# Kernel tuning notes

Measured on AMD Instinct MI355X. Metric: run time of the kernel, lower is better.

The kernel has to match this reference:

```python
import jax, jax.numpy as jnp
import numpy as np

B, CIN, COUT, H, W_ = 8, 48, 64, 224, 224
KS, PAD = 3, 1
BN_EPS = 1e-5
TWO_PI = 2.0 * np.pi


def _ste(hard, soft):
    # forward value = hard, gradient flows through soft
    return soft + jax.lax.stop_gradient(hard - soft)


def channel_adaptive_bypass(x, out_ch):
    in_ch = x.shape[1]
    repeat, merge = out_ch // in_ch, out_ch % in_ch
    b, _, h, w = x.shape
    parts = []
    if repeat > 0:
        parts.append(jnp.tile(x, (1, repeat, 1, 1)))
    if merge > 0:
        regular = in_ch // merge * (merge - 1)
        parts.append(x[:, :regular].reshape(b, -1, merge - 1, h, w).mean(axis=1))
        parts.append(x[:, regular:].reshape(b, -1, 1, h, w).mean(axis=1))
    return jnp.concatenate(parts, axis=1)


def setup_inputs() -> dict:
    key = jax.random.key(0)
    ks = jax.random.split(key, 2)
    x = jax.random.normal(ks[0], (B, CIN, H, W_), dtype=jnp.float32)
    weight = 0.001 * jax.random.normal(ks[1], (COUT, CIN, KS, KS), dtype=jnp.float32)
    return {
        'x': x,
        'alpha': jnp.ones((1,), jnp.float32),
        'epsilon': jnp.zeros((1, CIN, 1, 1), jnp.float32),
        'tau': jnp.ones((1, CIN, 1, 1), jnp.float32),
        'A': jnp.ones((1, CIN, 1, 1), jnp.float32),
        'weight': weight,
        'gamma': jnp.ones((COUT,), jnp.float32),
        'beta': jnp.zeros((COUT,), jnp.float32),
    }


def reference(x, alpha, epsilon, tau, A, weight, gamma, beta):
    inp = x
    # PeriodicBinarizer: sin-based periodic binarization with tanh STE
    z = (x - epsilon) / tau * TWO_PI
    s = jnp.sin(z)
    xa = _ste(jnp.sign(s), jnp.tanh(s * alpha)) * A
    # BinaryWeightConv2d: per-filter mean-|w| scaled sign weights, clip STE
    scale = jax.lax.stop_gradient(jnp.mean(jnp.abs(weight), axis=(1, 2, 3), keepdims=True))
    bw = _ste(scale * jnp.sign(weight), jnp.clip(weight, -1.0, 1.0))
    y = jax.lax.conv_general_dilated(
        xa, bw, window_strides=(1, 1), padding=((PAD, PAD), (PAD, PAD)),
        dimension_numbers=('NCHW', 'OIHW', 'NCHW'))
    # BatchNorm2d (training mode: batch statistics, biased variance)
    mu = jnp.mean(y, axis=(0, 2, 3), keepdims=True)
    var = jnp.var(y, axis=(0, 2, 3), keepdims=True)
    yn = (y - mu) * jax.lax.rsqrt(var + BN_EPS)
    yn = yn * gamma[None, :, None, None] + beta[None, :, None, None]
    return yn + channel_adaptive_bypass(inp, COUT)
```

## Files before the change

### kernel.cpp

```cpp
#include <hip/hip_runtime.h>
#include <math.h>

#define BB   8
#define CI   48
#define CO   64
#define HH   224
#define WW   224
#define HW   50176
#define NPC  (BB*HW)
#define HP   226
#define WP   226
#define PADW (HP*WP)

typedef unsigned long long u64;
typedef unsigned int u32;

constexpr float TWO_PI_F = 6.283185307179586476925286766559f;

constexpr size_t YOFF  = 0;
constexpr size_t XBOFF = YOFF  + (size_t)BB*CO*HW*2;
constexpr size_t WBOFF = XBOFF + (size_t)BB*PADW*8;
constexpr size_t S2OFF = WBOFF + (size_t)CO*9*8;
constexpr size_t CROFF = S2OFF + CO*8;
constexpr size_t SAOFF = CROFF + 9*CO*4;
constexpr size_t S1OFF = SAOFF + CO*4;

static_assert(S2OFF % 8 == 0, "S2 must be 8B-aligned for u64 atomicAdd");

__global__ __launch_bounds__(64) void k_prep(const float* __restrict__ w,
                                             const float* __restrict__ A,
                                             u64* __restrict__ wb, float* __restrict__ sA,
                                             int* __restrict__ corr,
                                             int* __restrict__ S1, u64* __restrict__ S2) {
    const int o = blockIdx.x;
    const int i = threadIdx.x;
    float wv[9];
    double acc = 0.0;
    if (i < CI) {
        #pragma unroll
        for (int k = 0; k < 9; ++k) {
            wv[k] = w[(size_t)(o * CI + i) * 9 + k];
            acc += fabs((double)wv[k]);
        }
    } else {
        #pragma unroll
        for (int k = 0; k < 9; ++k) wv[k] = 0.0f;
    }
    #pragma unroll
    for (int m = 32; m > 0; m >>= 1) acc += __shfl_xor(acc, m, 64);
    u64 bits[9];
    int wpop[9];
    #pragma unroll
    for (int k = 0; k < 9; ++k) {
        bits[k] = __ballot(i < CI && wv[k] > 0.0f);
        wpop[k] = __popcll(bits[k]);
    }
    if (i == 0) {
        sA[o] = (float)(acc / 432.0) * A[0];
        S1[o] = 0;
        S2[o] = 0ull;
        #pragma unroll
        for (int k = 0; k < 9; ++k) wb[o * 9 + k] = bits[k];
    }
    if (i < 9) {
        const int rc = i / 3, cc = i - rc * 3;
        int nv = 0, ws = 0;
        #pragma unroll
        for (int k = 0; k < 9; ++k) {
            const int r = k / 3, kc = k - r * 3;
            const bool inv = (rc == 0 && r == 0) || (rc == 2 && r == 2) ||
                             (cc == 0 && kc == 0) || (cc == 2 && kc == 2);
            if (inv) ws += wpop[k]; else ++nv;
        }
        corr[i * CO + o] = 48 * nv + 2 * ws;
    }
}

__global__ __launch_bounds__(256) void k_pack(const float* __restrict__ x,
                                              const float* __restrict__ eps,
                                              const float* __restrict__ tau,
                                              u64* __restrict__ xbp) {
    const int t = blockIdx.x * 256 + threadIdx.x;
    if (t < BB * 900) {
        const int b = t / 900, j = t - b * 900;
        int r, c;
        if (j < 226)      { r = 0;             c = j; }
        else if (j < 452) { r = 225;           c = j - 226; }
        else if (j < 676) { r = 1 + (j - 452); c = 0; }
        else              { r = 1 + (j - 676); c = 225; }
        xbp[(size_t)b * PADW + r * WP + c] = 0ull;
    }
    const int b = t / HW;
    const int p = t - b * HW;
    const int h = p / WW, w = p - h * WW;
    const float* xp = x + (size_t)b * CI * HW + p;
    u64 w0 = 0;
    for (int c = 0; c < CI; ++c) {
        const float v = xp[(size_t)c * HW];
        if (sinf((v - eps[c]) / tau[c] * TWO_PI_F) > 0.0f) w0 |= (1ull << c);
    }
    xbp[(size_t)b * PADW + (size_t)(h + 1) * WP + (w + 1)] = w0;
}

__global__ __launch_bounds__(256) void k_conv(const u64* __restrict__ xbp,
                                              const u64* __restrict__ wbg,
                                              const int* __restrict__ corrg,
                                              short* __restrict__ y) {
    __shared__ u64 wbs[CO * 9];
    __shared__ int cs[9 * CO];
    const int tid = threadIdx.x;
    for (int i = tid; i < CO * 9; i += 256) wbs[i] = wbg[i];
    for (int i = tid; i < 9 * CO; i += 256) cs[i] = corrg[i];
    __syncthreads();

    const int t = blockIdx.x * 256 + tid;
    const int b = t / (HW / 2);
    const int pr = t - b * (HW / 2);
    const int p = pr * 2;
    const int h = p / WW, w = p - h * WW;

    const u64* xp = xbp + (size_t)b * PADW + (size_t)h * WP + w;
    u64 win[3][4];
    #pragma unroll
    for (int r = 0; r < 3; ++r)
        #pragma unroll
        for (int c = 0; c < 4; ++c)
            win[r][c] = xp[r * WP + c];

    const int rc  = (h == 0) ? 0 : ((h == HH - 1) ? 2 : 1);
    const int ci0 = (rc * 3 + ((w == 0) ? 0 : 1)) * CO;
    const int ci1 = (rc * 3 + ((w + 1 == WW - 1) ? 2 : 1)) * CO;

    short* yp = y + (size_t)b * CO * HW + p;
    #pragma unroll 2
    for (int o = 0; o < CO; ++o) {
        const u64* wo = &wbs[o * 9];
        int d0 = 0, d1 = 0;
        #pragma unroll
        for (int r = 0; r < 3; ++r) {
            #pragma unroll
            for (int k = 0; k < 3; ++k) {
                const u64 wk = wo[r * 3 + k];
                d0 += __popcll(win[r][k] ^ wk);
                d1 += __popcll(win[r][k + 1] ^ wk);
            }
        }
        const int cnt0 = cs[ci0 + o] - 2 * d0;
        const int cnt1 = cs[ci1 + o] - 2 * d1;
        *(short2*)(yp + (size_t)o * HW) = make_short2((short)cnt0, (short)cnt1);
    }
}

__global__ __launch_bounds__(256) void k_stats(const short* __restrict__ y,
                                               int* __restrict__ S1,
                                               u64* __restrict__ S2) {
    const int o = blockIdx.x >> 3;
    const int part = blockIdx.x & 7;
    const int tid = threadIdx.x;
    int s1 = 0;
    u32 s2 = 0;
    for (int b = 0; b < BB; ++b) {
        const int4* yp = (const int4*)(y + ((size_t)b * CO + o) * HW);
        for (int v = part * 784 + tid; v < (part + 1) * 784; v += 256) {
            const int4 q = yp[v];
            int u;
            u = q.x; { const int a = (u << 16) >> 16, c = u >> 16; s1 += a + c; s2 += (u32)(a*a + c*c); }
            u = q.y; { const int a = (u << 16) >> 16, c = u >> 16; s1 += a + c; s2 += (u32)(a*a + c*c); }
            u = q.z; { const int a = (u << 16) >> 16, c = u >> 16; s1 += a + c; s2 += (u32)(a*a + c*c); }
            u = q.w; { const int a = (u << 16) >> 16, c = u >> 16; s1 += a + c; s2 += (u32)(a*a + c*c); }
        }
    }
    __shared__ long long r1[256];
    __shared__ long long r2[256];
    r1[tid] = s1;
    r2[tid] = (long long)s2;
    __syncthreads();
    for (int st = 128; st > 0; st >>= 1) {
        if (tid < st) { r1[tid] += r1[tid + st]; r2[tid] += r2[tid + st]; }
        __syncthreads();
    }
    if (tid == 0) {
        atomicAdd(&S1[o], (int)r1[0]);
        atomicAdd((unsigned long long*)&S2[o], (u64)r2[0]);
    }
}

__global__ __launch_bounds__(256) void k_final(const float* __restrict__ x,
                                               const short* __restrict__ y,
                                               const int* __restrict__ S1,
                                               const u64* __restrict__ S2,
                                               const float* __restrict__ sA,
                                               const float* __restrict__ gam,
                                               const float* __restrict__ bta,
                                               float* __restrict__ out) {
    __shared__ float sh[2];
    const int o = blockIdx.y, b = blockIdx.z;
    if (threadIdx.x == 0) {
        const double m1 = (double)S1[o] / (double)NPC;
        const double m2 = (double)(long long)S2[o] / (double)NPC;
        const double vr = m2 - m1 * m1;
        const float s = sA[o];
        const float var = (float)((double)s * (double)s * vr);
        const float inv = (float)(1.0 / sqrt((double)var + (double)1e-5f));
        sh[0] = s * inv * gam[o];
        sh[1] = bta[o] - (float)(s * m1) * inv * gam[o];
    }
    __syncthreads();
    const float ca = sh[0], cb = sh[1];

    const int p = blockIdx.x * 1024 + threadIdx.x * 4;
    const short4 yv = *(const short4*)(y + ((size_t)b * CO + o) * HW + p);
    float4 r;
    r.x = fmaf(ca, (float)yv.x, cb);
    r.y = fmaf(ca, (float)yv.y, cb);
    r.z = fmaf(ca, (float)yv.z, cb);
    r.w = fmaf(ca, (float)yv.w, cb);

    const float* xb_ = x + (size_t)b * CI * HW + p;
    if (o < CI) {
        const float4 xv = *(const float4*)(xb_ + (size_t)o * HW);
        r.x += xv.x; r.y += xv.y; r.z += xv.z; r.w += xv.w;
    } else {
        const int j = o - CI;
        const int c0 = (j < 15) ? j      : 45;
        const int c1 = (j < 15) ? j + 15 : 46;
        const int c2 = (j < 15) ? j + 30 : 47;
        const float4 x0 = *(const float4*)(xb_ + (size_t)c0 * HW);
        const float4 x1 = *(const float4*)(xb_ + (size_t)c1 * HW);
        const float4 x2 = *(const float4*)(xb_ + (size_t)c2 * HW);
        r.x += (x0.x + x1.x + x2.x) * (1.0f / 3.0f);
        r.y += (x0.y + x1.y + x2.y) * (1.0f / 3.0f);
        r.z += (x0.z + x1.z + x2.z) * (1.0f / 3.0f);
        r.w += (x0.w + x1.w + x2.w) * (1.0f / 3.0f);
    }
    *(float4*)(out + ((size_t)b * CO + o) * HW + p) = r;
}

extern "C" void kernel_launch(void* const* d_in, const int* in_sizes, int n_in,
                              void* d_out, int out_size, void* d_ws, size_t ws_size,
                              hipStream_t stream) {
    const float* x     = (const float*)d_in[0];
    const float* eps   = (const float*)d_in[2];
    const float* tau   = (const float*)d_in[3];
    const float* A     = (const float*)d_in[4];
    const float* w     = (const float*)d_in[5];
    const float* gamma = (const float*)d_in[6];
    const float* beta  = (const float*)d_in[7];
    float* out = (float*)d_out;

    char* ws = (char*)d_ws;
    short* y    = (short*)(ws + YOFF);
    u64*   xbp  = (u64*)(ws + XBOFF);
    u64*   wb   = (u64*)(ws + WBOFF);
    u64*   S2   = (u64*)(ws + S2OFF);
    int*   corr = (int*)(ws + CROFF);
    float* sA   = (float*)(ws + SAOFF);
    int*   S1   = (int*)(ws + S1OFF);

    k_prep <<<CO, 64, 0, stream>>>(w, A, wb, sA, corr, S1, S2);
    k_pack <<<NPC / 256, 256, 0, stream>>>(x, eps, tau, xbp);
    k_conv <<<NPC / 2 / 256, 256, 0, stream>>>(xbp, wb, corr, y);
    k_stats<<<CO * 8, 256, 0, stream>>>(y, S1, S2);
    k_final<<<dim3(HW / 1024, CO, BB), 256, 0, stream>>>(x, y, S1, S2, sA, gamma, beta, out);
}
```

Baseline: 278.5 us.

## Fuse BN statistics into binary conv and pack two pixels per thread

Removes the separate statistics kernel by accumulating per-channel sum and sum of squares inside the conv kernel, using shared-memory atomics spread over 32 slots and then one global atomic per channel per block. This avoids re-reading the int16 conv output from memory. The pack kernel also now handles two adjacent pixels per thread with float2 loads, halving its grid. The cost is two shared atomics per output channel per thread in the conv inner loop, plus extra shared memory that may reduce occupancy.

```diff
diff --git a/kernel.cpp b/kernel.cpp
--- a/kernel.cpp
+++ b/kernel.cpp
@@ -90,27 +90,41 @@
         else              { r = 1 + (j - 676); c = 225; }
         xbp[(size_t)b * PADW + r * WP + c] = 0ull;
     }
-    const int b = t / HW;
-    const int p = t - b * HW;
+    const int b = t / (HW / 2);
+    const int pr = t - b * (HW / 2);
+    const int p = pr * 2;
     const int h = p / WW, w = p - h * WW;
-    const float* xp = x + (size_t)b * CI * HW + p;
-    u64 w0 = 0;
+    u64 w0 = 0, w1 = 0;
     for (int c = 0; c < CI; ++c) {
-        const float v = xp[(size_t)c * HW];
-        if (sinf((v - eps[c]) / tau[c] * TWO_PI_F) > 0.0f) w0 |= (1ull << c);
-    }
-    xbp[(size_t)b * PADW + (size_t)(h + 1) * WP + (w + 1)] = w0;
+        const float2 v = *(const float2*)(x + ((size_t)b * CI + c) * HW + p);
+        const float e = eps[c], tu = tau[c];
+        const u64 bit = 1ull << c;
+        if (sinf((v.x - e) / tu * TWO_PI_F) > 0.0f) w0 |= bit;
+        if (sinf((v.y - e) / tu * TWO_PI_F) > 0.0f) w1 |= bit;
+    }
+    u64* d = xbp + (size_t)b * PADW + (size_t)(h + 1) * WP + (w + 1);
+    d[0] = w0;
+    d[1] = w1;
 }
 
 __global__ __launch_bounds__(256) void k_conv(const u64* __restrict__ xbp,
                                               const u64* __restrict__ wbg,
                                               const int* __restrict__ corrg,
-                                              short* __restrict__ y) {
+                                              short* __restrict__ y,
+                                              int* __restrict__ S1,
+                                              u64* __restrict__ S2) {
     __shared__ u64 wbs[CO * 9];
     __shared__ int cs[9 * CO];
+    __shared__ int ls1[CO][32];
+    __shared__ u32 ls2[CO][32];
     const int tid = threadIdx.x;
     for (int i = tid; i < CO * 9; i += 256) wbs[i] = wbg[i];
     for (int i = tid; i < 9 * CO; i += 256) cs[i] = corrg[i];
+    {
+        int* z1 = &ls1[0][0];
+        u32* z2 = &ls2[0][0];
+        for (int i = tid; i < CO * 32; i += 256) { z1[i] = 0; z2[i] = 0u; }
+    }
     __syncthreads();
 
     const int t = blockIdx.x * 256 + tid;
@@ -131,6 +145,7 @@
     const int ci0 = (rc * 3 + ((w == 0) ? 0 : 1)) * CO;
     const int ci1 = (rc * 3 + ((w + 1 == WW - 1) ? 2 : 1)) * CO;
 
+    const int slot = tid & 31;
     short* yp = y + (size_t)b * CO * HW + p;
     #pragma unroll 2
     for (int o = 0; o < CO; ++o) {
@@ -148,40 +163,17 @@
         const int cnt0 = cs[ci0 + o] - 2 * d0;
         const int cnt1 = cs[ci1 + o] - 2 * d1;
         *(short2*)(yp + (size_t)o * HW) = make_short2((short)cnt0, (short)cnt1);
-    }
-}
-
-__global__ __launch_bounds__(256) void k_stats(const short* __restrict__ y,
-                                               int* __restrict__ S1,
-                                               u64* __restrict__ S2) {
-    const int o = blockIdx.x >> 3;
-    const int part = blockIdx.x & 7;
-    const int tid = threadIdx.x;
-    int s1 = 0;
-    u32 s2 = 0;
-    for (int b = 0; b < BB; ++b) {
-        const int4* yp = (const int4*)(y + ((size_t)b * CO + o) * HW);
-        for (int v = part * 784 + tid; v < (part + 1) * 784; v += 256) {
-            const int4 q = yp[v];
-            int u;
-            u = q.x; { const int a = (u << 16) >> 16, c = u >> 16; s1 += a + c; s2 += (u32)(a*a + c*c); }
-            u = q.y; { const int a = (u << 16) >> 16, c = u >> 16; s1 += a + c; s2 += (u32)(a*a + c*c); }
-            u = q.z; { const int a = (u << 16) >> 16, c = u >> 16; s1 += a + c; s2 += (u32)(a*a + c*c); }
-            u = q.w; { const int a = (u << 16) >> 16, c = u >> 16; s1 += a + c; s2 += (u32)(a*a + c*c); }
-        }
-    }
-    __shared__ long long r1[256];
-    __shared__ long long r2[256];
-    r1[tid] = s1;
-    r2[tid] = (long long)s2;
+        atomicAdd(&ls1[o][slot], cnt0 + cnt1);
+        atomicAdd(&ls2[o][slot], (u32)(cnt0 * cnt0 + cnt1 * cnt1));
+    }
     __syncthreads();
-    for (int st = 128; st > 0; st >>= 1) {
-        if (tid < st) { r1[tid] += r1[tid + st]; r2[tid] += r2[tid + st]; }
-        __syncthreads();
-    }
-    if (tid == 0) {
-        atomicAdd(&S1[o], (int)r1[0]);
-        atomicAdd((unsigned long long*)&S2[o], (u64)r2[0]);
+    if (tid < CO) {
+        int s1 = 0;
+        u32 s2 = 0;
+        #pragma unroll
+        for (int s = 0; s < 32; ++s) { s1 += ls1[tid][s]; s2 += ls2[tid][s]; }
+        atomicAdd(&S1[tid], s1);
+        atomicAdd((unsigned long long*)&S2[tid], (u64)s2);
     }
 }
 
@@ -258,8 +250,7 @@
     int*   S1   = (int*)(ws + S1OFF);
 
     k_prep <<<CO, 64, 0, stream>>>(w, A, wb, sA, corr, S1, S2);
-    k_pack <<<NPC / 256, 256, 0, stream>>>(x, eps, tau, xbp);
-    k_conv <<<NPC / 2 / 256, 256, 0, stream>>>(xbp, wb, corr, y);
-    k_stats<<<CO * 8, 256, 0, stream>>>(y, S1, S2);
+    k_pack <<<NPC / 2 / 256, 256, 0, stream>>>(x, eps, tau, xbp);
+    k_conv <<<NPC / 2 / 256, 256, 0, stream>>>(xbp, wb, corr, y, S1, S2);
     k_final<<<dim3(HW / 1024, CO, BB), 256, 0, stream>>>(x, y, S1, S2, sA, gamma, beta, out);
 }
```

After: 275.2 us. Within noise of the previous version (-1.2%).
